# Kernel tuning notes

Hardware: AMD Instinct MI355X
Metric: run time of the kernel (lower is better)

Reference implementation:

```python
import jax, jax.numpy as jnp
import numpy as np


def setup_inputs() -> dict:
    key = jax.random.key(0)
    k1, k2, k3 = jax.random.split(key, 3)
    B, C, L, D = 2, 8, 256, 128
    start_hidden = jax.random.normal(k1, (B, C, L, D), dtype=jnp.float32)
    end_hidden = jax.random.normal(k2, (B, C, L, D), dtype=jnp.float32)
    # nn.Parameter initialized uniform_(-0.1, 0.1)
    v = jax.random.uniform(k3, (D,), dtype=jnp.float32, minval=-0.1, maxval=0.1)
    return {"start_hidden": start_hidden, "end_hidden": end_hidden, "v": v}


def reference(start_hidden, end_hidden, v):
    # start_hidden: [B, C, L, D], end_hidden: [B, C, L, D], v: [D]
    # additive pairwise scoring: tanh(s_i + e_j) . v  for every (i, j) span
    add_hidden = jnp.tanh(start_hidden[:, :, :, None, :] + end_hidden[:, :, None, :, :])  # [B,C,L,L,D]
    res = jnp.einsum('bcnmd,d->bcnm', add_hidden, v)  # [B, C, L, L]
    span_ner_mat_tensor = jnp.transpose(res, (0, 2, 3, 1))  # [B, L, L, C]
    return span_ner_mat_tensor
```

## Files before the change

kernel.cpp:

```cpp
#include <hip/hip_runtime.h>


#define LDIM 256
#define DDIM 128
#define DPAD 132

__global__ __launch_bounds__(256) void span_tanh_dot_kernel(
    const float* __restrict__ start_h,
    const float* __restrict__ end_h,
    const float* __restrict__ v,
    float* __restrict__ out,
    int C)
{
    __shared__ float s_pool[32 * DPAD];
    __shared__ float e_t[32][DPAD];
    __shared__ float s_vsum;
    float (*s_t)[DPAD] = (float (*)[DPAD])s_pool;

    const int bc = blockIdx.z;
    const int i0 = blockIdx.y * 32;
    const int j0 = blockIdx.x * 32;
    const int tx = threadIdx.x;
    const int ty = threadIdx.y;
    const int g  = threadIdx.z;
    const int t  = ty * 8 + tx;
    const int tid = g * 64 + t;

    const float K = 2.8853900817779268f;

    const float* sg = start_h + ((size_t)bc * LDIM + i0) * DDIM;
    const float* eg = end_h   + ((size_t)bc * LDIM + j0) * DDIM;

    #pragma unroll
    for (int k = 0; k < 4; ++k) {
        const int idx = tid + k * 256;
        const int r  = idx >> 5;
        const int c4 = (idx & 31) << 2;
        float4 a = *(const float4*)(sg + r * DDIM + c4);
        a.x = __builtin_amdgcn_exp2f(K * a.x);
        a.y = __builtin_amdgcn_exp2f(K * a.y);
        a.z = __builtin_amdgcn_exp2f(K * a.z);
        a.w = __builtin_amdgcn_exp2f(K * a.w);
        *(float4*)(&s_t[r][c4]) = a;
        float4 b = *(const float4*)(eg + r * DDIM + c4);
        b.x = __builtin_amdgcn_exp2f(K * b.x);
        b.y = __builtin_amdgcn_exp2f(K * b.y);
        b.z = __builtin_amdgcn_exp2f(K * b.z);
        b.w = __builtin_amdgcn_exp2f(K * b.w);
        *(float4*)(&e_t[r][c4]) = b;
    }

    if (g == 0) {
        float2 vv = *(const float2*)(v + 2 * t);
        float p = vv.x + vv.y;
        #pragma unroll
        for (int off = 1; off < 64; off <<= 1) p += __shfl_xor(p, off);
        if (t == 0) s_vsum = p;
    }
    __syncthreads();

    const int dbase = __builtin_amdgcn_readfirstlane(g) * 32;

    float acc00 = 0.f, acc01 = 0.f, acc02 = 0.f, acc03 = 0.f;
    float acc10 = 0.f, acc11 = 0.f, acc12 = 0.f, acc13 = 0.f;
    float acc20 = 0.f, acc21 = 0.f, acc22 = 0.f, acc23 = 0.f;
    float acc30 = 0.f, acc31 = 0.f, acc32 = 0.f, acc33 = 0.f;

#define QUAD(ACC, S, E)                                            \
    {                                                              \
        float q0 = fmaf((S).x, (E).x, 1.0f);                       \
        float q1 = fmaf((S).y, (E).y, 1.0f);                       \
        float q2 = fmaf((S).z, (E).z, 1.0f);                       \
        float q3 = fmaf((S).w, (E).w, 1.0f);                       \
        float ab = q0 * q1, cd = q2 * q3;                          \
        float n01 = fmaf(v0, q1, v1 * q0);                         \
        float n23 = fmaf(v2, q3, v3 * q2);                         \
        float N = fmaf(n01, cd, n23 * ab);                         \
        float r = __builtin_amdgcn_rcpf(ab * cd);                  \
        ACC = fmaf(N, r, ACC);                                     \
    }

    #pragma unroll 2
    for (int it = 0; it < 8; ++it) {
        const int d = dbase + it * 4;
        const float4 s0 = *(const float4*)(&s_t[ty     ][d]);
        const float4 s1 = *(const float4*)(&s_t[ty +  8][d]);
        const float4 s2 = *(const float4*)(&s_t[ty + 16][d]);
        const float4 s3 = *(const float4*)(&s_t[ty + 24][d]);
        const float4 e0 = *(const float4*)(&e_t[tx     ][d]);
        const float4 e1 = *(const float4*)(&e_t[tx +  8][d]);
        const float4 e2 = *(const float4*)(&e_t[tx + 16][d]);
        const float4 e3 = *(const float4*)(&e_t[tx + 24][d]);
        const float v0 = v[d], v1 = v[d + 1], v2 = v[d + 2], v3 = v[d + 3];

        QUAD(acc00, s0, e0); QUAD(acc01, s0, e1); QUAD(acc02, s0, e2); QUAD(acc03, s0, e3);
        QUAD(acc10, s1, e0); QUAD(acc11, s1, e1); QUAD(acc12, s1, e2); QUAD(acc13, s1, e3);
        QUAD(acc20, s2, e0); QUAD(acc21, s2, e1); QUAD(acc22, s2, e2); QUAD(acc23, s2, e3);
        QUAD(acc30, s3, e0); QUAD(acc31, s3, e1); QUAD(acc32, s3, e2); QUAD(acc33, s3, e3);
    }
#undef QUAD

    __syncthreads();
    float* red = s_pool;
#define PARK(A, B, ACC) red[(((A) * 4 + (B)) * 4 + g) * 64 + t] = ACC;
    PARK(0,0,acc00) PARK(0,1,acc01) PARK(0,2,acc02) PARK(0,3,acc03)
    PARK(1,0,acc10) PARK(1,1,acc11) PARK(1,2,acc12) PARK(1,3,acc13)
    PARK(2,0,acc20) PARK(2,1,acc21) PARK(2,2,acc22) PARK(2,3,acc23)
    PARK(3,0,acc30) PARK(3,1,acc31) PARK(3,2,acc32) PARK(3,3,acc33)
#undef PARK
    __syncthreads();

#define COMB(B)                                                    \
    (red[((g * 4 + (B)) * 4 + 0) * 64 + t] +                       \
     red[((g * 4 + (B)) * 4 + 1) * 64 + t] +                       \
     red[((g * 4 + (B)) * 4 + 2) * 64 + t] +                       \
     red[((g * 4 + (B)) * 4 + 3) * 64 + t])
    const float o0 = COMB(0);
    const float o1 = COMB(1);
    const float o2 = COMB(2);
    const float o3 = COMB(3);
#undef COMB

    const int b_ = bc / C;
    const int c_ = bc - b_ * C;
    const float Sv = s_vsum;
    const int i = i0 + ty + 8 * g;
    const size_t rowbase = (((size_t)b_ * LDIM + i) * LDIM) * C + c_;
    out[rowbase + (size_t)(j0 + tx     ) * C] = fmaf(-2.f, o0, Sv);
    out[rowbase + (size_t)(j0 + tx +  8) * C] = fmaf(-2.f, o1, Sv);
    out[rowbase + (size_t)(j0 + tx + 16) * C] = fmaf(-2.f, o2, Sv);
    out[rowbase + (size_t)(j0 + tx + 24) * C] = fmaf(-2.f, o3, Sv);
}

extern "C" void kernel_launch(void* const* d_in, const int* in_sizes, int n_in,
                              void* d_out, int out_size, void* d_ws, size_t ws_size,
                              hipStream_t stream) {
    const float* start_h = (const float*)d_in[0];
    const float* end_h   = (const float*)d_in[1];
    const float* v       = (const float*)d_in[2];
    float* out = (float*)d_out;

    const int BC = in_sizes[0] / (LDIM * DDIM);
    const int C  = 8;

    dim3 grid(LDIM / 32, LDIM / 32, BC);
    dim3 block(8, 8, 4);
    span_tanh_dot_kernel<<<grid, block, 0, stream>>>(start_h, end_h, v, out, C);
}
```

Baseline: 19.04 us.

## Store exp tiles as bf16 and fold v weights into rational tanh terms

The exponentiated start and end tiles are now stored in shared memory as bf16, which halves LDS footprint and read traffic. Each start element is pre-scaled by -1/(2v_d), so every term becomes 1/(s*e + w) and the per-quad numerator simplifies to additions instead of v-weighted FMAs. This cuts VALU work in the inner loop. It costs bf16 precision loss, and the reciprocal of v blows up when v is near zero, which risks accuracy and even inf or nan.

```diff
diff --git a/kernel.cpp b/kernel.cpp
--- a/kernel.cpp
+++ b/kernel.cpp
@@ -3,7 +3,18 @@
 
 #define LDIM 256
 #define DDIM 128
-#define DPAD 132
+#define DPADH 136
+
+__device__ __forceinline__ unsigned bf1(float x) {
+    unsigned u = __float_as_uint(x);
+    u += 0x7FFFu + ((u >> 16) & 1u);
+    return u >> 16;
+}
+__device__ __forceinline__ unsigned pack2(float x, float y) {
+    return bf1(x) | (bf1(y) << 16);
+}
+__device__ __forceinline__ float lo16(unsigned u) { return __uint_as_float(u << 16); }
+__device__ __forceinline__ float hi16(unsigned u) { return __uint_as_float(u & 0xFFFF0000u); }
 
 __global__ __launch_bounds__(256) void span_tanh_dot_kernel(
     const float* __restrict__ start_h,
@@ -12,10 +23,11 @@
     float* __restrict__ out,
     int C)
 {
-    __shared__ float s_pool[32 * DPAD];
-    __shared__ float e_t[32][DPAD];
+    __shared__ float pool[4096];
+    __shared__ unsigned short e_t[32][DPADH];
+    __shared__ float W_s[DDIM];
     __shared__ float s_vsum;
-    float (*s_t)[DPAD] = (float (*)[DPAD])s_pool;
+    unsigned short (*s_t)[DPADH] = (unsigned short (*)[DPADH])pool;
 
     const int bc = blockIdx.z;
     const int i0 = blockIdx.y * 32;
@@ -31,23 +43,57 @@
     const float* sg = start_h + ((size_t)bc * LDIM + i0) * DDIM;
     const float* eg = end_h   + ((size_t)bc * LDIM + j0) * DDIM;
 
+    if (tid < 32) {
+        const float4 vv = *(const float4*)(v + 4 * tid);
+        float4 w;
+        w.x = -0.5f * __builtin_amdgcn_rcpf(vv.x);
+        w.y = -0.5f * __builtin_amdgcn_rcpf(vv.y);
+        w.z = -0.5f * __builtin_amdgcn_rcpf(vv.z);
+        w.w = -0.5f * __builtin_amdgcn_rcpf(vv.w);
+        *(float4*)(&W_s[4 * tid]) = w;
+    }
+
     #pragma unroll
-    for (int k = 0; k < 4; ++k) {
+    for (int k = 0; k < 2; ++k) {
         const int idx = tid + k * 256;
-        const int r  = idx >> 5;
-        const int c4 = (idx & 31) << 2;
-        float4 a = *(const float4*)(sg + r * DDIM + c4);
-        a.x = __builtin_amdgcn_exp2f(K * a.x);
-        a.y = __builtin_amdgcn_exp2f(K * a.y);
-        a.z = __builtin_amdgcn_exp2f(K * a.z);
-        a.w = __builtin_amdgcn_exp2f(K * a.w);
-        *(float4*)(&s_t[r][c4]) = a;
-        float4 b = *(const float4*)(eg + r * DDIM + c4);
-        b.x = __builtin_amdgcn_exp2f(K * b.x);
-        b.y = __builtin_amdgcn_exp2f(K * b.y);
-        b.z = __builtin_amdgcn_exp2f(K * b.z);
-        b.w = __builtin_amdgcn_exp2f(K * b.w);
-        *(float4*)(&e_t[r][c4]) = b;
+        const int r  = idx >> 4;
+        const int c8 = (idx & 15) << 3;
+        const float4 va = *(const float4*)(v + c8);
+        const float4 vb = *(const float4*)(v + c8 + 4);
+        const float w0 = -0.5f * __builtin_amdgcn_rcpf(va.x);
+        const float w1 = -0.5f * __builtin_amdgcn_rcpf(va.y);
+        const float w2 = -0.5f * __builtin_amdgcn_rcpf(va.z);
+        const float w3 = -0.5f * __builtin_amdgcn_rcpf(va.w);
+        const float w4 = -0.5f * __builtin_amdgcn_rcpf(vb.x);
+        const float w5 = -0.5f * __builtin_amdgcn_rcpf(vb.y);
+        const float w6 = -0.5f * __builtin_amdgcn_rcpf(vb.z);
+        const float w7 = -0.5f * __builtin_amdgcn_rcpf(vb.w);
+
+        float4 a0 = *(const float4*)(sg + r * DDIM + c8);
+        float4 a1 = *(const float4*)(sg + r * DDIM + c8 + 4);
+        uint4 ps;
+        ps.x = pack2(__builtin_amdgcn_exp2f(K * a0.x) * w0,
+                     __builtin_amdgcn_exp2f(K * a0.y) * w1);
+        ps.y = pack2(__builtin_amdgcn_exp2f(K * a0.z) * w2,
+                     __builtin_amdgcn_exp2f(K * a0.w) * w3);
+        ps.z = pack2(__builtin_amdgcn_exp2f(K * a1.x) * w4,
+                     __builtin_amdgcn_exp2f(K * a1.y) * w5);
+        ps.w = pack2(__builtin_amdgcn_exp2f(K * a1.z) * w6,
+                     __builtin_amdgcn_exp2f(K * a1.w) * w7);
+        *(uint4*)(&s_t[r][c8]) = ps;
+
+        float4 b0 = *(const float4*)(eg + r * DDIM + c8);
+        float4 b1 = *(const float4*)(eg + r * DDIM + c8 + 4);
+        uint4 pe;
+        pe.x = pack2(__builtin_amdgcn_exp2f(K * b0.x),
+                     __builtin_amdgcn_exp2f(K * b0.y));
+        pe.y = pack2(__builtin_amdgcn_exp2f(K * b0.z),
+                     __builtin_amdgcn_exp2f(K * b0.w));
+        pe.z = pack2(__builtin_amdgcn_exp2f(K * b1.x),
+                     __builtin_amdgcn_exp2f(K * b1.y));
+        pe.w = pack2(__builtin_amdgcn_exp2f(K * b1.z),
+                     __builtin_amdgcn_exp2f(K * b1.w));
+        *(uint4*)(&e_t[r][c8]) = pe;
     }
 
     if (g == 0) {
@@ -59,49 +105,91 @@
     }
     __syncthreads();
 
-    const int dbase = __builtin_amdgcn_readfirstlane(g) * 32;
+    const int d0 = __builtin_amdgcn_readfirstlane(g) * 32;
 
     float acc00 = 0.f, acc01 = 0.f, acc02 = 0.f, acc03 = 0.f;
     float acc10 = 0.f, acc11 = 0.f, acc12 = 0.f, acc13 = 0.f;
     float acc20 = 0.f, acc21 = 0.f, acc22 = 0.f, acc23 = 0.f;
     float acc30 = 0.f, acc31 = 0.f, acc32 = 0.f, acc33 = 0.f;
 
-#define QUAD(ACC, S, E)                                            \
-    {                                                              \
-        float q0 = fmaf((S).x, (E).x, 1.0f);                       \
-        float q1 = fmaf((S).y, (E).y, 1.0f);                       \
-        float q2 = fmaf((S).z, (E).z, 1.0f);                       \
-        float q3 = fmaf((S).w, (E).w, 1.0f);                       \
-        float ab = q0 * q1, cd = q2 * q3;                          \
-        float n01 = fmaf(v0, q1, v1 * q0);                         \
-        float n23 = fmaf(v2, q3, v3 * q2);                         \
-        float N = fmaf(n01, cd, n23 * ab);                         \
-        float r = __builtin_amdgcn_rcpf(ab * cd);                  \
-        ACC = fmaf(N, r, ACC);                                     \
-    }
-
-    #pragma unroll 2
-    for (int it = 0; it < 8; ++it) {
-        const int d = dbase + it * 4;
-        const float4 s0 = *(const float4*)(&s_t[ty     ][d]);
-        const float4 s1 = *(const float4*)(&s_t[ty +  8][d]);
-        const float4 s2 = *(const float4*)(&s_t[ty + 16][d]);
-        const float4 s3 = *(const float4*)(&s_t[ty + 24][d]);
-        const float4 e0 = *(const float4*)(&e_t[tx     ][d]);
-        const float4 e1 = *(const float4*)(&e_t[tx +  8][d]);
-        const float4 e2 = *(const float4*)(&e_t[tx + 16][d]);
-        const float4 e3 = *(const float4*)(&e_t[tx + 24][d]);
-        const float v0 = v[d], v1 = v[d + 1], v2 = v[d + 2], v3 = v[d + 3];
-
-        QUAD(acc00, s0, e0); QUAD(acc01, s0, e1); QUAD(acc02, s0, e2); QUAD(acc03, s0, e3);
-        QUAD(acc10, s1, e0); QUAD(acc11, s1, e1); QUAD(acc12, s1, e2); QUAD(acc13, s1, e3);
-        QUAD(acc20, s2, e0); QUAD(acc21, s2, e1); QUAD(acc22, s2, e2); QUAD(acc23, s2, e3);
-        QUAD(acc30, s3, e0); QUAD(acc31, s3, e1); QUAD(acc32, s3, e2); QUAD(acc33, s3, e3);
+#define UNPACK8(U, P)                                                  \
+    const float P##0 = lo16((U).x), P##1 = hi16((U).x),                \
+                P##2 = lo16((U).y), P##3 = hi16((U).y),                \
+                P##4 = lo16((U).z), P##5 = hi16((U).z),                \
+                P##6 = lo16((U).w), P##7 = hi16((U).w);
+
+#define QUAD(ACC, A0, A1, A2, A3, B0, B1, B2, B3, WV)                  \
+    {                                                                  \
+        float uu0 = fmaf(A0, B0, (WV).x);                              \
+        float uu1 = fmaf(A1, B1, (WV).y);                              \
+        float uu2 = fmaf(A2, B2, (WV).z);                              \
+        float uu3 = fmaf(A3, B3, (WV).w);                              \
+        float pab = uu0 * uu1, pcd = uu2 * uu3;                        \
+        float pn01 = uu0 + uu1;                                        \
+        float pn23 = uu2 + uu3;                                        \
+        float pN = fmaf(pn01, pcd, pn23 * pab);                        \
+        float prr = __builtin_amdgcn_rcpf(pab * pcd);                  \
+        ACC = fmaf(pN, prr, ACC);                                      \
+    }
+
+    #pragma unroll
+    for (int it = 0; it < 4; ++it) {
+        const int d = d0 + it * 8;
+        const uint4 SU0 = *(const uint4*)(&s_t[ty     ][d]);
+        const uint4 SU1 = *(const uint4*)(&s_t[ty +  8][d]);
+        const uint4 SU2 = *(const uint4*)(&s_t[ty + 16][d]);
+        const uint4 SU3 = *(const uint4*)(&s_t[ty + 24][d]);
+        const uint4 EU0 = *(const uint4*)(&e_t[tx     ][d]);
+        const uint4 EU1 = *(const uint4*)(&e_t[tx +  8][d]);
+        const uint4 EU2 = *(const uint4*)(&e_t[tx + 16][d]);
+        const uint4 EU3 = *(const uint4*)(&e_t[tx + 24][d]);
+        const float4 Wa = *(const float4*)(&W_s[d]);
+        const float4 Wb = *(const float4*)(&W_s[d + 4]);
+
+        UNPACK8(SU0, sA) UNPACK8(SU1, sB) UNPACK8(SU2, sC) UNPACK8(SU3, sD)
+        UNPACK8(EU0, eA) UNPACK8(EU1, eB) UNPACK8(EU2, eC) UNPACK8(EU3, eD)
+
+        QUAD(acc00, sA0,sA1,sA2,sA3, eA0,eA1,eA2,eA3, Wa);
+        QUAD(acc00, sA4,sA5,sA6,sA7, eA4,eA5,eA6,eA7, Wb);
+        QUAD(acc01, sA0,sA1,sA2,sA3, eB0,eB1,eB2,eB3, Wa);
+        QUAD(acc01, sA4,sA5,sA6,sA7, eB4,eB5,eB6,eB7, Wb);
+        QUAD(acc02, sA0,sA1,sA2,sA3, eC0,eC1,eC2,eC3, Wa);
+        QUAD(acc02, sA4,sA5,sA6,sA7, eC4,eC5,eC6,eC7, Wb);
+        QUAD(acc03, sA0,sA1,sA2,sA3, eD0,eD1,eD2,eD3, Wa);
+        QUAD(acc03, sA4,sA5,sA6,sA7, eD4,eD5,eD6,eD7, Wb);
+
+        QUAD(acc10, sB0,sB1,sB2,sB3, eA0,eA1,eA2,eA3, Wa);
+        QUAD(acc10, sB4,sB5,sB6,sB7, eA4,eA5,eA6,eA7, Wb);
+        QUAD(acc11, sB0,sB1,sB2,sB3, eB0,eB1,eB2,eB3, Wa);
+        QUAD(acc11, sB4,sB5,sB6,sB7, eB4,eB5,eB6,eB7, Wb);
+        QUAD(acc12, sB0,sB1,sB2,sB3, eC0,eC1,eC2,eC3, Wa);
+        QUAD(acc12, sB4,sB5,sB6,sB7, eC4,eC5,eC6,eC7, Wb);
+        QUAD(acc13, sB0,sB1,sB2,sB3, eD0,eD1,eD2,eD3, Wa);
+        QUAD(acc13, sB4,sB5,sB6,sB7, eD4,eD5,eD6,eD7, Wb);
+
+        QUAD(acc20, sC0,sC1,sC2,sC3, eA0,eA1,eA2,eA3, Wa);
+        QUAD(acc20, sC4,sC5,sC6,sC7, eA4,eA5,eA6,eA7, Wb);
+        QUAD(acc21, sC0,sC1,sC2,sC3, eB0,eB1,eB2,eB3, Wa);
+        QUAD(acc21, sC4,sC5,sC6,sC7, eB4,eB5,eB6,eB7, Wb);
+        QUAD(acc22, sC0,sC1,sC2,sC3, eC0,eC1,eC2,eC3, Wa);
+        QUAD(acc22, sC4,sC5,sC6,sC7, eC4,eC5,eC6,eC7, Wb);
+        QUAD(acc23, sC0,sC1,sC2,sC3, eD0,eD1,eD2,eD3, Wa);
+        QUAD(acc23, sC4,sC5,sC6,sC7, eD4,eD5,eD6,eD7, Wb);
+
+        QUAD(acc30, sD0,sD1,sD2,sD3, eA0,eA1,eA2,eA3, Wa);
+        QUAD(acc30, sD4,sD5,sD6,sD7, eA4,eA5,eA6,eA7, Wb);
+        QUAD(acc31, sD0,sD1,sD2,sD3, eB0,eB1,eB2,eB3, Wa);
+        QUAD(acc31, sD4,sD5,sD6,sD7, eB4,eB5,eB6,eB7, Wb);
+        QUAD(acc32, sD0,sD1,sD2,sD3, eC0,eC1,eC2,eC3, Wa);
+        QUAD(acc32, sD4,sD5,sD6,sD7, eC4,eC5,eC6,eC7, Wb);
+        QUAD(acc33, sD0,sD1,sD2,sD3, eD0,eD1,eD2,eD3, Wa);
+        QUAD(acc33, sD4,sD5,sD6,sD7, eD4,eD5,eD6,eD7, Wb);
     }
 #undef QUAD
+#undef UNPACK8
 
     __syncthreads();
-    float* red = s_pool;
+    float* red = pool;
 #define PARK(A, B, ACC) red[(((A) * 4 + (B)) * 4 + g) * 64 + t] = ACC;
     PARK(0,0,acc00) PARK(0,1,acc01) PARK(0,2,acc02) PARK(0,3,acc03)
     PARK(1,0,acc10) PARK(1,1,acc11) PARK(1,2,acc12) PARK(1,3,acc13)
@@ -126,10 +214,10 @@
     const float Sv = s_vsum;
     const int i = i0 + ty + 8 * g;
     const size_t rowbase = (((size_t)b_ * LDIM + i) * LDIM) * C + c_;
-    out[rowbase + (size_t)(j0 + tx     ) * C] = fmaf(-2.f, o0, Sv);
-    out[rowbase + (size_t)(j0 + tx +  8) * C] = fmaf(-2.f, o1, Sv);
-    out[rowbase + (size_t)(j0 + tx + 16) * C] = fmaf(-2.f, o2, Sv);
-    out[rowbase + (size_t)(j0 + tx + 24) * C] = fmaf(-2.f, o3, Sv);
+    out[rowbase + (size_t)(j0 + tx     ) * C] = Sv + o0;
+    out[rowbase + (size_t)(j0 + tx +  8) * C] = Sv + o1;
+    out[rowbase + (size_t)(j0 + tx + 16) * C] = Sv + o2;
+    out[rowbase + (size_t)(j0 + tx + 24) * C] = Sv + o3;
 }
 
 extern "C" void kernel_launch(void* const* d_in, const int* in_sizes, int n_in,
```

Measured after the change: 24.16 us. +26.9%, slower.
